# Performance work log

Measured on AMD Instinct MI355X. Metric: run time of the kernel, lower is better.

## Reference

```python
import jax, jax.numpy as jnp
import jax.scipy.linalg as jsl
import numpy as np

B, T, C = 2, 4096, 1024
HK = HV = 8           # linear_num_key_heads == linear_num_value_heads
DK = DV = 128         # linear_key_head_dim / linear_value_head_dim
CHUNK = 64
CONV_K = 4
KEY_DIM = HK * DK
VAL_DIM = HV * DV
CONV_DIM = 2 * KEY_DIM + VAL_DIM
EPS = 1e-6


def setup_inputs() -> dict:
    key = jax.random.key(0)
    ks = jax.random.split(key, 8)
    s = 0.02
    x = jax.random.normal(ks[0], (B, T, C), jnp.float32)
    W_qkvz = jax.random.normal(ks[1], (C, 2 * KEY_DIM + 2 * VAL_DIM), jnp.float32) * s
    W_ba = jax.random.normal(ks[2], (C, 2 * HV), jnp.float32) * s
    conv_w = jax.random.normal(ks[3], (CONV_DIM, 1, CONV_K), jnp.float32) * 0.3  # depthwise (O,1,K)
    dt_bias = jnp.ones((HV,), jnp.float32)
    A_log = jnp.log(jax.random.uniform(ks[4], (HV,), jnp.float32, 0.5, 8.0))
    norm_weight = jnp.ones((DV,), jnp.float32)
    W_out = jax.random.normal(ks[5], (VAL_DIM, C), jnp.float32) * s
    return {"x": x, "W_qkvz": W_qkvz, "W_ba": W_ba, "conv_w": conv_w,
            "dt_bias": dt_bias, "A_log": A_log, "norm_weight": norm_weight, "W_out": W_out}


def _l2norm(x, eps=EPS):
    return x * jax.lax.rsqrt(jnp.sum(x * x, -1, keepdims=True) + eps)


def _chunk_gated_delta_rule(q, k, v, g, beta, chunk=CHUNK):
    # q,k: (B,T,H,DK); v: (B,T,H,DV); g,beta: (B,T,H)
    q = _l2norm(q)
    k = _l2norm(k)
    tr = lambda x: jnp.swapaxes(x, 1, 2).astype(jnp.float32)  # -> (B,H,T,...)
    q, k, v, g, beta = tr(q), tr(k), tr(v), tr(g), tr(beta)
    b, h, t, dk = k.shape
    dv = v.shape[-1]
    n = t // chunk  # T divisible by chunk (pad_size == 0)
    q = q * (dk ** -0.5)
    v_beta = v * beta[..., None]
    k_beta = k * beta[..., None]
    rs = lambda x: x.reshape(b, h, n, chunk, x.shape[-1])
    q, k, v_beta, k_beta = rs(q), rs(k), rs(v_beta), rs(k_beta)
    g = jnp.cumsum(g.reshape(b, h, n, chunk), axis=-1)
    # decay_mask[..., i, j] = exp(g_i - g_j) for j <= i, else 0
    decay = jnp.tril(jnp.exp(jnp.tril(g[..., :, None] - g[..., None, :])))
    # forward substitution == unit-lower-triangular solve: (I + tri)^{-1}
    tri = jnp.tril(jnp.einsum('bhnck,bhndk->bhncd', k_beta, k) * decay, -1)
    eye = jnp.eye(chunk, dtype=jnp.float32)
    Tm = jsl.solve_triangular(eye + tri, jnp.broadcast_to(eye, tri.shape), lower=True)
    v_new = Tm @ v_beta                                   # (B,H,N,C,DV)
    k_cum = Tm @ (k_beta * jnp.exp(g)[..., None])         # (B,H,N,C,DK)
    keep_low = jnp.tril(jnp.ones((chunk, chunk), bool))

    def step(S, inp):
        q_i, k_i, v_i, kc_i, g_i, dm_i = inp              # (B,H,C,*)
        attn = jnp.where(keep_low, (q_i @ jnp.swapaxes(k_i, -1, -2)) * dm_i, 0.0)
        v_n = v_i - kc_i @ S
        out = (q_i * jnp.exp(g_i)[..., None]) @ S + attn @ v_n
        g_last = g_i[..., -1]
        S = S * jnp.exp(g_last)[..., None, None] + jnp.einsum(
            'bhck,bhcv->bhkv', k_i * jnp.exp(g_last[..., None] - g_i)[..., None], v_n)
        return S, out

    mv = lambda x: jnp.moveaxis(x, 2, 0)                  # chunk axis to front
    S0 = jnp.zeros((b, h, dk, dv), jnp.float32)
    S, outs = jax.lax.scan(step, S0, (mv(q), mv(k), mv(v_new), mv(k_cum), mv(g), mv(decay)))
    out = jnp.moveaxis(outs, 0, 2).reshape(b, h, t, dv)
    return jnp.swapaxes(out, 1, 2), S                     # (B,T,H,DV), (B,H,DK,DV)


def reference(x, W_qkvz, W_ba, conv_w, dt_bias, A_log, norm_weight, W_out):
    Bx, Tx, Cx = x.shape
    ratio = HV // HK
    qkvz = (x @ W_qkvz).reshape(Bx, Tx, HK, 2 * DK + 2 * ratio * DV)
    q, k, v, z = jnp.split(qkvz, [DK, 2 * DK, 2 * DK + ratio * DV], axis=3)
    v = v.reshape(Bx, Tx, HV, DV)
    z = z.reshape(Bx, Tx, HV, DV)
    ba = (x @ W_ba).reshape(Bx, Tx, HK, 2 * ratio)
    b_, a_ = jnp.split(ba, [ratio], axis=3)
    b_ = b_.reshape(Bx, Tx, HV)
    a_ = a_.reshape(Bx, Tx, HV)
    mixed = jnp.concatenate([q.reshape(Bx, Tx, -1), k.reshape(Bx, Tx, -1),
                             v.reshape(Bx, Tx, -1)], axis=-1)
    # causal depthwise conv1d (left pad K-1, take first T)
    xc = jnp.swapaxes(mixed, 1, 2)                        # (B, CONV_DIM, T)
    conv = jax.lax.conv_general_dilated(xc, conv_w, (1,), [(CONV_K - 1, 0)],
                                        dimension_numbers=('NCH', 'OIH', 'NCH'),
                                        feature_group_count=CONV_DIM)
    conv = jnp.swapaxes(jax.nn.silu(conv), 1, 2)          # (B,T,CONV_DIM)
    qc, kc, vc = jnp.split(conv, [KEY_DIM, 2 * KEY_DIM], axis=-1)
    qc = qc.reshape(Bx, Tx, HK, DK)
    kc = kc.reshape(Bx, Tx, HK, DK)
    vc = vc.reshape(Bx, Tx, HV, DV)
    if ratio > 1:
        qc = jnp.repeat(qc, ratio, axis=2)
        kc = jnp.repeat(kc, ratio, axis=2)
    beta = jax.nn.sigmoid(b_)
    g = -jnp.exp(A_log) * jax.nn.softplus(a_ + dt_bias)
    core, _ = _chunk_gated_delta_rule(qc, kc, vc, g, beta)
    # GatedRMSNorm over head_v_dim, gated by silu(z)
    h = core.astype(jnp.float32)
    var = jnp.mean(h * h, -1, keepdims=True)
    h = norm_weight * (h * jax.lax.rsqrt(var + EPS))
    h = h * jax.nn.silu(z.astype(jnp.float32))
    return h.reshape(Bx, Tx, VAL_DIM) @ W_out
```

## Files before the change

kernel.cpp:

```cpp
#include <hip/hip_runtime.h>
#include <cstddef>

#define Bx 2
#define Tn 4096
#define Hh 8

typedef unsigned short u16;
typedef unsigned int u32;
typedef __attribute__((ext_vector_type(8))) short short8;
typedef __attribute__((ext_vector_type(4))) float f32x4;

__device__ __forceinline__ float bf2f(u16 u) {
  u32 x = ((u32)u) << 16;
  return __uint_as_float(x);
}
__device__ __forceinline__ u16 f2bf(float f) {
  u32 x = __float_as_uint(f);
  u32 lsb = (x >> 16) & 1;
  x += 0x7fffu + lsb;
  return (u16)(x >> 16);
}
__device__ __forceinline__ u32 pack2(float a, float b) {
  return (u32)f2bf(a) | ((u32)f2bf(b) << 16);
}
__device__ __forceinline__ short8 cvt8(float4 f0, float4 f1) {
  uint4 p;
  p.x = pack2(f0.x, f0.y);
  p.y = pack2(f0.z, f0.w);
  p.z = pack2(f1.x, f1.y);
  p.w = pack2(f1.z, f1.w);
  return *(short8*)&p;
}
__device__ __forceinline__ void async16(u16* lds, const u16* g) {
  __builtin_amdgcn_global_load_lds((const __attribute__((address_space(1))) void*)g,
                                   (__attribute__((address_space(3))) void*)lds, 16, 0, 0);
}

__global__ __launch_bounds__(256) void conv_bf16(const float* __restrict__ X,
                                                 u16* __restrict__ Xb) {
  int i = (blockIdx.x * 256 + threadIdx.x) * 8;
  float4 v0 = *(const float4*)&X[i];
  float4 v1 = *(const float4*)&X[i + 4];
  uint4 pv;
  pv.x = pack2(v0.x, v0.y);
  pv.y = pack2(v0.z, v0.w);
  pv.z = pack2(v1.x, v1.y);
  pv.w = pack2(v1.z, v1.w);
  *(uint4*)&Xb[i] = pv;
}

__global__ __launch_bounds__(256) void transpose_bf16(const float* __restrict__ W,
                                                      u16* __restrict__ WT,
                                                      int K, int N) {
  __shared__ float tile[64][68];
  int nb = blockIdx.x, kb = blockIdx.y;
  int tid = threadIdx.x;
  int r = tid >> 4, c4 = (tid & 15) * 4;
#pragma unroll
  for (int p = 0; p < 4; p++) {
    int k = kb * 64 + p * 16 + r;
    float4 v = *(const float4*)&W[(size_t)k * N + nb * 64 + c4];
    tile[p * 16 + r][c4] = v.x;
    tile[p * 16 + r][c4 + 1] = v.y;
    tile[p * 16 + r][c4 + 2] = v.z;
    tile[p * 16 + r][c4 + 3] = v.w;
  }
  __syncthreads();
  int rn = tid >> 2, ck = (tid & 3) * 16;
#pragma unroll
  for (int s = 0; s < 2; s++) {
    int k0 = ck + s * 8;
    uint4 pv;
    pv.x = pack2(tile[k0 + 0][rn], tile[k0 + 1][rn]);
    pv.y = pack2(tile[k0 + 2][rn], tile[k0 + 3][rn]);
    pv.z = pack2(tile[k0 + 4][rn], tile[k0 + 5][rn]);
    pv.w = pack2(tile[k0 + 6][rn], tile[k0 + 7][rn]);
    *(uint4*)&WT[(size_t)(nb * 64 + rn) * K + kb * 64 + k0] = pv;
  }
}

__global__ __launch_bounds__(512, 1) void gemm_qkvz(const u16* __restrict__ A,
                                                    const u16* __restrict__ Bt,
                                                    u16* __restrict__ O1,
                                                    u16* __restrict__ O2) {
  const int K = 1024;
  extern __shared__ __align__(16) u16 gl[];
  int lin = blockIdx.x;
  int sl = (lin & 7) * 64 + (lin >> 3);
  int bm = sl & 31;
  int bn = sl >> 5;
  int tid = threadIdx.x;
  int wid = tid >> 6, lane = tid & 63;
  int wm = wid >> 2, wn = wid & 3;
  int m_lane = lane & 15, kgrp = lane >> 4, m7 = m_lane & 7;

  f32x4 acc[8][4];
#pragma unroll
  for (int i = 0; i < 8; i++)
#pragma unroll
    for (int j = 0; j < 4; j++) acc[i][j] = (f32x4){0.f, 0.f, 0.f, 0.f};

  int srow = lane >> 3;
  int gc8 = ((lane & 7) ^ srow) * 8;
  const u16* Ab = A + (size_t)(bm * 256 + wid * 32 + srow) * K + gc8;
  const u16* Bb = Bt + (size_t)(bn * 256 + wid * 32 + srow) * K + gc8;

#pragma unroll
  for (int i = 0; i < 4; i++) {
    async16(gl + (wid * 32 + i * 8) * 64, Ab + (size_t)(i * 8) * K);
    async16(gl + 32768 + (wid * 32 + i * 8) * 64, Bb + (size_t)(i * 8) * K);
  }
  asm volatile("s_waitcnt vmcnt(0)" ::: "memory");
  __builtin_amdgcn_s_barrier();

  for (int t = 0; t < 16; t++) {
    int p = t & 1;
    const u16* Ap = gl + p * 16384;
    const u16* Bp = gl + 32768 + p * 16384;
    if (t < 15) {
      int pn = p ^ 1;
      int kk = (t + 1) * 64;
#pragma unroll
      for (int i = 0; i < 4; i++) {
        async16(gl + pn * 16384 + (wid * 32 + i * 8) * 64, Ab + (size_t)(i * 8) * K + kk);
        async16(gl + 32768 + pn * 16384 + (wid * 32 + i * 8) * 64, Bb + (size_t)(i * 8) * K + kk);
      }
    }
    short8 bq[2][4];
#pragma unroll
    for (int ks = 0; ks < 2; ks++)
#pragma unroll
      for (int nf = 0; nf < 4; nf++)
        bq[ks][nf] = *(const short8*)&Bp[(wn * 64 + nf * 16 + m_lane) * 64 +
                                         (((ks * 4 + kgrp) ^ m7) << 3)];
#pragma unroll
    for (int mf = 0; mf < 8; mf++) {
      short8 aq0 = *(const short8*)&Ap[(wm * 128 + mf * 16 + m_lane) * 64 +
                                       ((kgrp ^ m7) << 3)];
      short8 aq1 = *(const short8*)&Ap[(wm * 128 + mf * 16 + m_lane) * 64 +
                                       (((4 + kgrp) ^ m7) << 3)];
#pragma unroll
      for (int nf = 0; nf < 4; nf++)
        acc[mf][nf] = __builtin_amdgcn_mfma_f32_16x16x32_bf16(aq0, bq[0][nf], acc[mf][nf], 0, 0, 0);
#pragma unroll
      for (int nf = 0; nf < 4; nf++)
        acc[mf][nf] = __builtin_amdgcn_mfma_f32_16x16x32_bf16(aq1, bq[1][nf], acc[mf][nf], 0, 0, 0);
    }
    if (t < 15) {
      asm volatile("s_waitcnt vmcnt(0) lgkmcnt(0)" ::: "memory");
      __builtin_amdgcn_s_barrier();
      __builtin_amdgcn_sched_barrier(0);
    }
  }

  int n0w = bn * 256 + wn * 64;
  int h = n0w >> 9, sub = (n0w >> 7) & 3;
  int cin = ((n0w & 127) & 64) + m_lane;
  u16* dst;
  size_t stride;
  if (sub < 3) { dst = O1 + (size_t)(sub * 1024 + h * 128); stride = 3072; }
  else         { dst = O2 + (size_t)(h * 128);              stride = 1024; }
  int rbase = bm * 256 + wm * 128 + kgrp * 4;
#pragma unroll
  for (int mf = 0; mf < 8; mf++)
#pragma unroll
    for (int nf = 0; nf < 4; nf++)
#pragma unroll
      for (int r = 0; r < 4; r++)
        dst[(size_t)(rbase + mf * 16 + r) * stride + cin + nf * 16] = f2bf(acc[mf][nf][r]);
}

template<int EPI>
__global__ __launch_bounds__(256) void gemm_mfma(const u16* __restrict__ A,
                                                 const u16* __restrict__ Bt,
                                                 u16* __restrict__ O1,
                                                 u16* __restrict__ O2,
                                                 float* __restrict__ O3,
                                                 int Nfull) {
  const int K = 1024;
  __shared__ u16 As[128 * 64];
  __shared__ u16 Bs[128 * 64];
  int lin = blockIdx.y * gridDim.x + blockIdx.x;
  int sl = lin >> 3;
  int cbn = gridDim.x >> 3;
  int bn = (lin & 7) * cbn + (sl % cbn);
  int bm = sl / cbn;
  int tid = threadIdx.x;
  int wave = tid >> 6, lane = tid & 63;
  int wr = wave >> 1, wc = wave & 1;

  f32x4 acc[4][4];
#pragma unroll
  for (int i = 0; i < 4; i++)
#pragma unroll
    for (int j = 0; j < 4; j++) acc[i][j] = (f32x4){0.f, 0.f, 0.f, 0.f};

  int srow = lane >> 3;
  int gc8 = ((lane & 7) ^ srow) * 8;
  const u16* Ab = A + (size_t)(bm * 128 + wave * 32 + srow) * K + gc8;
  const u16* Bb = Bt + (size_t)(bn * 128 + wave * 32 + srow) * K + gc8;
  u16* AsW = &As[(wave * 32) * 64];
  u16* BsW = &Bs[(wave * 32) * 64];

  int m_lane = lane & 15, kgrp = lane >> 4;
  int m7 = m_lane & 7;

  for (int kk = 0; kk < K; kk += 64) {
    __syncthreads();
#pragma unroll
    for (int i = 0; i < 4; i++) {
      async16(AsW + i * 512, Ab + (size_t)(i * 8) * K + kk);
      async16(BsW + i * 512, Bb + (size_t)(i * 8) * K + kk);
    }
    __syncthreads();
    short8 a[4][2], b[4][2];
#pragma unroll
    for (int t = 0; t < 4; t++)
#pragma unroll
      for (int ks = 0; ks < 2; ks++) {
        a[t][ks] = *(const short8*)&As[(wr * 64 + t * 16 + m_lane) * 64 +
                                       (((ks * 4 + kgrp) ^ m7) << 3)];
        b[t][ks] = *(const short8*)&Bs[(wc * 64 + t * 16 + m_lane) * 64 +
                                       (((ks * 4 + kgrp) ^ m7) << 3)];
      }
#pragma unroll
    for (int ks = 0; ks < 2; ks++)
#pragma unroll
      for (int i = 0; i < 4; i++)
#pragma unroll
        for (int j = 0; j < 4; j++)
          acc[i][j] = __builtin_amdgcn_mfma_f32_16x16x32_bf16(a[i][ks], b[j][ks],
                                                              acc[i][j], 0, 0, 0);
  }

  int n0 = bn * 128;
  int cbase = wc * 64 + (lane & 15);
  int rbase = bm * 128 + wr * 64 + ((lane >> 4) * 4);
  if (EPI == 1) {
    int h = n0 >> 9, sub = (n0 >> 7) & 3;
    u16* dst;
    size_t stride;
    if (sub < 3) { dst = O1 + (size_t)(sub * 1024 + h * 128); stride = 3072; }
    else         { dst = O2 + (size_t)(h * 128);              stride = 1024; }
#pragma unroll
    for (int i = 0; i < 4; i++)
#pragma unroll
      for (int j = 0; j < 4; j++)
#pragma unroll
        for (int r = 0; r < 4; r++)
          dst[(size_t)(rbase + i * 16 + r) * stride + cbase + j * 16] = f2bf(acc[i][j][r]);
  } else {
#pragma unroll
    for (int i = 0; i < 4; i++)
#pragma unroll
      for (int j = 0; j < 4; j++)
#pragma unroll
        for (int r = 0; r < 4; r++)
          O3[(size_t)(rbase + i * 16 + r) * Nfull + n0 + cbase + j * 16] = acc[i][j][r];
  }
}

__global__ __launch_bounds__(128) void ba_kernel(const float* __restrict__ x,
                                                 const float* __restrict__ Wba,
                                                 const float* __restrict__ dtb,
                                                 const float* __restrict__ Alog,
                                                 float* __restrict__ betab,
                                                 float* __restrict__ gb) {
  __shared__ float xs[1024];
  __shared__ float part[8][16];
  int row = blockIdx.x, tid = threadIdx.x;
#pragma unroll
  for (int r = 0; r < 2; r++) {
    int f4 = r * 128 + tid;
    *(float4*)&xs[f4 * 4] = *(const float4*)&x[(size_t)row * 1024 + f4 * 4];
  }
  __syncthreads();
  int col = tid & 15, seg = tid >> 4;
  float a = 0.f;
  for (int k = seg * 128; k < seg * 128 + 128; k++) a += xs[k] * Wba[k * 16 + col];
  part[seg][col] = a;
  __syncthreads();
  if (tid < 8) {
    float bval = 0.f, aval = 0.f;
#pragma unroll
    for (int q = 0; q < 8; q++) { bval += part[q][tid * 2]; aval += part[q][tid * 2 + 1]; }
    betab[(size_t)row * 8 + tid] = 1.f / (1.f + expf(-bval));
    float spin = aval + dtb[tid];
    float sp = (spin > 20.f) ? spin : log1pf(expf(spin));
    gb[(size_t)row * 8 + tid] = -expf(Alog[tid]) * sp;
  }
}

__global__ __launch_bounds__(256) void convnorm(const u16* __restrict__ mixed,
                                                const float* __restrict__ cw,
                                                const float* __restrict__ gbuf,
                                                u16* __restrict__ qn,
                                                u16* __restrict__ kn,
                                                u16* __restrict__ kdT,
                                                u16* __restrict__ vbT) {
  __shared__ __align__(16) u16 sRaw[67 * 128];
  __shared__ __align__(16) u16 sO[64 * 136];
  __shared__ float red_s[256];
  __shared__ float inv_s[64];
  __shared__ float eglc_s[64];
  int n = blockIdx.x, bh = blockIdx.y, type = blockIdx.z;
  int b = bh >> 3, h = bh & 7;
  int t0 = n * 64, tid = threadIdx.x;
  int srow = tid >> 4, scol8 = (tid & 15) * 8;
  int base = type << 10;

#pragma unroll
  for (int pass = 0; pass < 5; pass++) {
    int r = pass * 16 + srow;
    if (r < 67) {
      int t = t0 - 3 + r;
      uint4 v = make_uint4(0u, 0u, 0u, 0u);
      if (t >= 0) v = *(const uint4*)&mixed[(size_t)(b * Tn + t) * 3072 + base + h * 128 + scol8];
      *(uint4*)&sRaw[r * 128 + scol8] = v;
    }
  }
  if (type == 1 && tid < 64) {
    float gv = gbuf[(size_t)(b * Tn + t0 + tid) * 8 + h];
#pragma unroll
    for (int off = 1; off < 64; off <<= 1) {
      float o = __shfl_up(gv, off, 64);
      if (tid >= off) gv += o;
    }
    float gl = __shfl(gv, 63, 64);
    eglc_s[tid] = expf(gl - gv);
  }
  __syncthreads();

#pragma unroll
  for (int it = 0; it < 32; it++) {
    int idx = it * 256 + tid;
    int i = idx >> 7, d = idx & 127;
    int colw = (base + h * 128 + d) * 4;
    float a = 0.f;
#pragma unroll
    for (int tap = 0; tap < 4; tap++)
      a += bf2f(sRaw[(i + tap) * 128 + d]) * cw[colw + tap];
    a = a / (1.f + expf(-a));
    sO[i * 136 + d] = f2bf(a);
  }
  __syncthreads();

  if (type == 2) {
    const size_t tbase = (size_t)(bh * 64 + n) * 8192;
#pragma unroll
    for (int it = 0; it < 32; it++) {
      int idx = it * 256 + tid;
      int d = idx >> 6, i = idx & 63;
      vbT[tbase + d * 64 + i] = sO[i * 136 + d];
    }
    return;
  }

  {
    int i = tid >> 2, p = tid & 3;
    float ss = 0.f;
#pragma unroll
    for (int d = p * 32; d < p * 32 + 32; d += 2) {
      u32 w2 = *(const u32*)&sO[i * 136 + d];
      float a = bf2f(w2 & 0xffff), b2 = bf2f(w2 >> 16);
      ss += a * a + b2 * b2;
    }
    red_s[tid] = ss;
  }
  __syncthreads();
  if (tid < 64) {
    float inv = rsqrtf(red_s[tid * 4] + red_s[tid * 4 + 1] + red_s[tid * 4 + 2] + red_s[tid * 4 + 3] + 1e-6f);
    inv_s[tid] = (type == 0) ? inv * 0.08838834764831845f : inv;
  }
  __syncthreads();
  u16* dstRow = (type == 0 ? qn : kn) + (size_t)(bh * Tn + t0) * 128;
#pragma unroll
  for (int it = 0; it < 16; it++) {
    int idx = it * 256 + tid;
    int i = idx >> 6, d2 = (idx & 63) * 2;
    u32 w2 = *(const u32*)&sO[i * 136 + d2];
    float inv = inv_s[i];
    float q0 = bf2f(w2 & 0xffff) * inv, q1 = bf2f(w2 >> 16) * inv;
    u32 pk = pack2(q0, q1);
    if (type == 1) *(u32*)&sO[i * 136 + d2] = pk;
    *(u32*)&dstRow[(size_t)i * 128 + d2] = pk;
  }
  if (type == 1) {
    __syncthreads();
    const size_t tbase = (size_t)(bh * 64 + n) * 8192;
#pragma unroll
    for (int it = 0; it < 32; it++) {
      int idx = it * 256 + tid;
      int d = idx >> 6, i = idx & 63;
      kdT[tbase + d * 64 + i] = f2bf(bf2f(sO[i * 136 + d]) * eglc_s[i]);
    }
  }
}

__global__ __launch_bounds__(256) void prep(const float* __restrict__ gbuf,
                                            const float* __restrict__ betabuf,
                                            u16* qbuf,
                                            u16* kbuf,
                                            u16* vnT,
                                            u16* __restrict__ attn,
                                            float* __restrict__ egl) {
  __shared__ __align__(16) u16 sKn[64 * 136];
  __shared__ __align__(16) u16 sQn[64 * 136];
  __shared__ float gc_s[64], egc_s[64], bet_s[64];
  float* triL = (float*)sQn;

  int n = blockIdx.x, bh = blockIdx.y;
  int b = bh >> 3, h = bh & 7;
  int t0 = n * 64;
  int tid = threadIdx.x;
  const int rowg0 = b * Tn + t0;
  const int rowh0 = bh * Tn + t0;
  const size_t tbase = (size_t)(bh * 64 + n) * 8192;

  int wv = tid >> 6, lane = tid & 63;
  int m16 = lane & 15, q8 = (lane >> 4) * 8, qr = (lane >> 4) * 4;

#pragma unroll
  for (int it = 0; it < 4; it++) {
    int idx = it * 256 + tid;
    int i = idx >> 4, c8 = (idx & 15) * 8;
    *(uint4*)&sQn[i * 136 + c8] = *(const uint4*)&qbuf[(size_t)(rowh0 + i) * 128 + c8];
    *(uint4*)&sKn[i * 136 + c8] = *(const uint4*)&kbuf[(size_t)(rowh0 + i) * 128 + c8];
  }
  if (tid < 64) {
    float gv = gbuf[(size_t)(rowg0 + tid) * 8 + h];
    float bv = betabuf[(size_t)(rowg0 + tid) * 8 + h];
#pragma unroll
    for (int off = 1; off < 64; off <<= 1) {
      float o = __shfl_up(gv, off, 64);
      if (tid >= off) gv += o;
    }
    float gl = __shfl(gv, 63, 64);
    gc_s[tid] = gv;
    egc_s[tid] = expf(gv);
    bet_s[tid] = bv;
    if (tid == 63) egl[bh * 64 + n] = expf(gl);
  }
  __syncthreads();

#pragma unroll
  for (int it = 0; it < 16; it++) {
    int idx = it * 256 + tid;
    int i = idx >> 6, d2 = (idx & 63) * 2;
    u32 w2 = *(const u32*)&sQn[i * 136 + d2];
    float e = egc_s[i];
    *(u32*)&qbuf[(size_t)(rowh0 + i) * 128 + d2] =
        pack2(bf2f(w2 & 0xffff) * e, bf2f(w2 >> 16) * e);
  }
  {
    short8 qa[4];
#pragma unroll
    for (int kt = 0; kt < 4; kt++)
      qa[kt] = *(const short8*)&sQn[(wv * 16 + m16) * 136 + kt * 32 + q8];
    u16* atp = attn + (size_t)(bh * 64 + n) * 4096;
#pragma unroll
    for (int jt = 0; jt < 4; jt++) {
      int j = jt * 16 + m16;
      if (jt <= wv) {
        f32x4 o = (f32x4){0.f, 0.f, 0.f, 0.f};
#pragma unroll
        for (int kt = 0; kt < 4; kt++) {
          short8 kb = *(const short8*)&sKn[(jt * 16 + m16) * 136 + kt * 32 + q8];
          o = __builtin_amdgcn_mfma_f32_16x16x32_bf16(qa[kt], kb, o, 0, 0, 0);
        }
#pragma unroll
        for (int r = 0; r < 4; r++) {
          int i = wv * 16 + qr + r;
          float val = (j <= i) ? o[r] * expf(gc_s[i] - gc_s[j]) : 0.f;
          atp[i * 64 + j] = f2bf(val);
        }
      } else {
#pragma unroll
        for (int r = 0; r < 4; r++) atp[(wv * 16 + qr + r) * 64 + j] = 0;
      }
    }
  }
  __syncthreads();
  {
    short8 ka[4];
#pragma unroll
    for (int kt = 0; kt < 4; kt++)
      ka[kt] = *(const short8*)&sKn[(wv * 16 + m16) * 136 + kt * 32 + q8];
#pragma unroll
    for (int jt = 0; jt < 4; jt++) {
      int j = jt * 16 + m16;
      if (jt <= wv) {
        f32x4 o = (f32x4){0.f, 0.f, 0.f, 0.f};
#pragma unroll
        for (int kt = 0; kt < 4; kt++) {
          short8 kb = *(const short8*)&sKn[(jt * 16 + m16) * 136 + kt * 32 + q8];
          o = __builtin_amdgcn_mfma_f32_16x16x32_bf16(ka[kt], kb, o, 0, 0, 0);
        }
#pragma unroll
        for (int r = 0; r < 4; r++) {
          int i = wv * 16 + qr + r;
          triL[i * 64 + j] = (j < i) ? bet_s[i] * expf(gc_s[i] - gc_s[j]) * o[r] : 0.f;
        }
      } else if (jt == wv + 1) {
#pragma unroll
        for (int r = 0; r < 4; r++) triL[(wv * 16 + qr + r) * 64 + j] = 0.f;
      }
    }
  }
  __syncthreads();

  {
    int mat = tid >> 7, c = tid & 127;
    float x[64];
    if (mat == 0) {
#pragma unroll
      for (int i = 0; i < 64; i++)
        x[i] = bf2f(sKn[i * 136 + c]) * bet_s[i] * egc_s[i];
    } else {
#pragma unroll
      for (int i8 = 0; i8 < 8; i8++) {
        short8 vv = *(const short8*)&vnT[tbase + c * 64 + i8 * 8];
#pragma unroll
        for (int j = 0; j < 8; j++)
          x[i8 * 8 + j] = bf2f((u16)vv[j]) * bet_s[i8 * 8 + j];
      }
    }
#pragma unroll
    for (int i = 1; i < 64; i++) {
      float s0 = 0.f, s1 = 0.f, s2 = 0.f, s3 = 0.f;
#pragma unroll
      for (int l4 = 0; l4 < (i + 3) / 4; l4++) {
        float4 t4 = *(float4*)&triL[i * 64 + l4 * 4];
        s0 += t4.x * x[l4 * 4 + 0];
        s1 += t4.y * x[l4 * 4 + 1];
        s2 += t4.z * x[l4 * 4 + 2];
        s3 += t4.w * x[l4 * 4 + 3];
      }
      x[i] = x[i] - ((s0 + s1) + (s2 + s3));
    }
    if (mat == 0) {
#pragma unroll
      for (int i = 0; i < 64; i++) kbuf[(size_t)(rowh0 + i) * 128 + c] = f2bf(-x[i]);
    } else {
#pragma unroll
      for (int i = 0; i < 64; i += 2)
        *(u32*)&vnT[tbase + c * 64 + i] = pack2(x[i], x[i + 1]);
    }
  }
}

__device__ __forceinline__ void stage_quarter(int w, u16* ldsb,
                                              const u16* __restrict__ qgc,
                                              const u16* __restrict__ kcc,
                                              const u16* __restrict__ ktc,
                                              const u16* __restrict__ atc,
                                              const u16* __restrict__ vtc,
                                              int lane) {
  int l8 = lane * 8;
  if (w == 0) {
#pragma unroll
    for (int i = 0; i < 16; i++) {
      int p = i * 512 + l8;
      async16(ldsb + 8192 + i * 512, kcc + (p ^ ((((p >> 7) & 15)) << 3)));
    }
  } else if (w == 1) {
#pragma unroll
    for (int i = 0; i < 16; i++) {
      int p = i * 512 + l8;
      async16(ldsb + 16384 + i * 512, ktc + (p ^ ((((p >> 6) & 7)) << 3)));
    }
  } else if (w == 2) {
#pragma unroll
    for (int i = 0; i < 16; i++) {
      int p = i * 512 + l8;
      async16(ldsb + i * 512, qgc + (p ^ ((((p >> 7) & 15)) << 3)));
    }
  } else {
#pragma unroll
    for (int i = 0; i < 8; i++) {
      int p = i * 512 + l8;
      async16(ldsb + 24576 + i * 512, atc + (p ^ ((((p >> 6) & 7)) << 3)));
    }
#pragma unroll
    for (int i = 0; i < 2; i++) {
      int p = i * 512 + l8;
      async16(ldsb + 28672 + i * 512, vtc + (p ^ ((((p >> 6) & 7)) << 3)));
    }
  }
}

__global__ __launch_bounds__(256, 1) void scan_mfma(const u16* __restrict__ qg,
                                                    const u16* __restrict__ kdT,
                                                    const u16* __restrict__ vnT,
                                                    const u16* __restrict__ kcum,
                                                    const u16* __restrict__ attn,
                                                    const float* __restrict__ egl,
                                                    float* __restrict__ core) {
  extern __shared__ __align__(16) u16 dyn[];
  __shared__ __align__(16) u16 STb[16 * 128];
  __shared__ __align__(16) u16 VNb[16 * 64];
  int blk = blockIdx.x;
  int bh = blk & 15, tile = blk >> 4;
  int dv0 = tile * 16;
  int b = bh >> 3, h = bh & 7;
  int tid = threadIdx.x;
  int w = tid >> 6, lane = tid & 63;
  int q = lane >> 4, col = lane & 15;
  int c7 = col & 7;
  int qh = q >> 1, ql = q & 1;

  for (int r = tid; r < 16 * 128 / 2; r += 256) ((u32*)STb)[r] = 0u;
  float egAll = egl[bh * 64 + lane];

  f32x4 st0 = (f32x4){0.f, 0.f, 0.f, 0.f};
  f32x4 st1 = (f32x4){0.f, 0.f, 0.f, 0.f};

  const u16* qg_base = qg + (size_t)bh * Tn * 128;
  const u16* kc_base = kcum + (size_t)bh * Tn * 128;
  const u16* kt_base = kdT + (size_t)bh * 64 * 8192;
  const u16* at_base = attn + (size_t)bh * 64 * 4096;
  const u16* vt_base = vnT + (size_t)bh * 64 * 8192 + dv0 * 64;

  stage_quarter(w, dyn, qg_base, kc_base, kt_base, at_base, vt_base, lane);
  asm volatile("s_waitcnt vmcnt(0)" ::: "memory");
  __syncthreads();

  for (int n = 0; n < 64; n++) {
    u16* buf = dyn + (n & 1) * 29696;

    short8 kcf[4], qgf[4], ktf[4], atf[2], sb[4];
    uint2 vtf;
#pragma unroll
    for (int kt = 0; kt < 4; kt++) {
      kcf[kt] = *(const short8*)&buf[8192 + (w * 16 + col) * 128 + (((kt * 4 + q) ^ col) << 3)];
      qgf[kt] = *(const short8*)&buf[(w * 16 + col) * 128 + (((kt * 4 + q) ^ col) << 3)];
      sb[kt] = *(const short8*)&STb[col * 128 + (((kt * 4 + q) ^ col) << 3)];
    }
#pragma unroll
    for (int kt2 = 0; kt2 < 2; kt2++) {
      atf[kt2] = *(const short8*)&buf[24576 + (w * 16 + col) * 64 + (((kt2 * 4 + q) ^ c7) << 3)];
#pragma unroll
      for (int t = 0; t < 2; t++)
        ktf[t * 2 + kt2] = *(const short8*)&buf[16384 + ((w * 2 + t) * 16 + col) * 64 +
                                                (((kt2 * 4 + q) ^ c7) << 3)];
    }
    vtf = *(const uint2*)&buf[28672 + col * 64 + (((w * 2 + qh) ^ c7) << 3) + ql * 4];

    if (n < 63) {
      stage_quarter(w, dyn + ((n + 1) & 1) * 29696,
                    qg_base + (size_t)(n + 1) * 8192,
                    kc_base + (size_t)(n + 1) * 8192,
                    kt_base + (size_t)(n + 1) * 8192,
                    at_base + (size_t)(n + 1) * 4096,
                    vt_base + (size_t)(n + 1) * 8192, lane);
    }
    float eg = __shfl(egAll, n, 64);

    {
      f32x4 a0;
      a0[0] = bf2f(vtf.x & 0xffff); a0[1] = bf2f(vtf.x >> 16);
      a0[2] = bf2f(vtf.y & 0xffff); a0[3] = bf2f(vtf.y >> 16);
#pragma unroll
      for (int kt = 0; kt < 4; kt++)
        a0 = __builtin_amdgcn_mfma_f32_16x16x32_bf16(kcf[kt], sb[kt], a0, 0, 0, 0);
      uint2 pk;
      pk.x = pack2(a0[0], a0[1]);
      pk.y = pack2(a0[2], a0[3]);
      *(uint2*)&VNb[col * 64 + (((w * 2 + qh) ^ c7) << 3) + ql * 4] = pk;
    }
    asm volatile("s_waitcnt lgkmcnt(0)" ::: "memory");
    __builtin_amdgcn_s_barrier();
    __builtin_amdgcn_sched_barrier(0);

    short8 vb[2];
#pragma unroll
    for (int kt2 = 0; kt2 < 2; kt2++)
      vb[kt2] = *(const short8*)&VNb[col * 64 + (((kt2 * 4 + q) ^ c7) << 3)];

    {
      f32x4 s0;
      s0[0] = st0[0] * eg; s0[1] = st0[1] * eg; s0[2] = st0[2] * eg; s0[3] = st0[3] * eg;
      s0 = __builtin_amdgcn_mfma_f32_16x16x32_bf16(ktf[0], vb[0], s0, 0, 0, 0);
      s0 = __builtin_amdgcn_mfma_f32_16x16x32_bf16(ktf[1], vb[1], s0, 0, 0, 0);
      st0 = s0;
      uint2 pk;
      pk.x = pack2(s0[0], s0[1]);
      pk.y = pack2(s0[2], s0[3]);
      *(uint2*)&STb[col * 128 + ((((w * 2 + 0) * 2 + qh) ^ col) << 3) + ql * 4] = pk;
    }
    {
      f32x4 s1;
      s1[0] = st1[0] * eg; s1[1] = st1[1] * eg; s1[2] = st1[2] * eg; s1[3] = st1[3] * eg;
      s1 = __builtin_amdgcn_mfma_f32_16x16x32_bf16(ktf[2], vb[0], s1, 0, 0, 0);
      s1 = __builtin_amdgcn_mfma_f32_16x16x32_bf16(ktf[3], vb[1], s1, 0, 0, 0);
      st1 = s1;
      uint2 pk;
      pk.x = pack2(s1[0], s1[1]);
      pk.y = pack2(s1[2], s1[3]);
      *(uint2*)&STb[col * 128 + ((((w * 2 + 1) * 2 + qh) ^ col) << 3) + ql * 4] = pk;
    }

    {
      f32x4 o = (f32x4){0.f, 0.f, 0.f, 0.f};
#pragma unroll
      for (int kt = 0; kt < 4; kt++)
        o = __builtin_amdgcn_mfma_f32_16x16x32_bf16(qgf[kt], sb[kt], o, 0, 0, 0);
#pragma unroll
      for (int kt2 = 0; kt2 < 2; kt2++)
        o = __builtin_amdgcn_mfma_f32_16x16x32_bf16(atf[kt2], vb[kt2], o, 0, 0, 0);
      size_t rowb = (size_t)(b * Tn) + n * 64 + w * 16 + q * 4;
#pragma unroll
      for (int r2 = 0; r2 < 4; r2++)
        core[(rowb + r2) * 1024 + h * 128 + dv0 + col] = o[r2];
    }

    asm volatile("s_waitcnt vmcnt(4) lgkmcnt(0)" ::: "memory");
    __builtin_amdgcn_s_barrier();
    __builtin_amdgcn_sched_barrier(0);
  }
}

__global__ __launch_bounds__(256) void gnorm(const float* __restrict__ core,
                                             const u16* __restrict__ z,
                                             const float* __restrict__ nw,
                                             u16* __restrict__ coreb) {
  __shared__ float red[256];
  __shared__ float rstd[8];
  int row = blockIdx.x, tid = threadIdx.x;
  float4 c4 = *(const float4*)&core[(size_t)row * 1024 + tid * 4];
  uint2 zl = *(const uint2*)&z[(size_t)row * 1024 + tid * 4];
  float4 z4;
  z4.x = bf2f(zl.x & 0xffff); z4.y = bf2f(zl.x >> 16);
  z4.z = bf2f(zl.y & 0xffff); z4.w = bf2f(zl.y >> 16);
  red[tid] = c4.x * c4.x + c4.y * c4.y + c4.z * c4.z + c4.w * c4.w;
  __syncthreads();
  if (tid < 8) {
    float s = 0.f;
    for (int t2 = tid * 32; t2 < tid * 32 + 32; t2++) s += red[t2];
    rstd[tid] = rsqrtf(s * (1.f / 128.f) + 1e-6f);
  }
  __syncthreads();
  float rs = rstd[tid >> 5];
  int d0 = (tid * 4) & 127;
  float4 w4 = *(const float4*)&nw[d0];
  float4 o;
  o.x = c4.x * rs * w4.x * (z4.x / (1.f + expf(-z4.x)));
  o.y = c4.y * rs * w4.y * (z4.y / (1.f + expf(-z4.y)));
  o.z = c4.z * rs * w4.z * (z4.z / (1.f + expf(-z4.z)));
  o.w = c4.w * rs * w4.w * (z4.w / (1.f + expf(-z4.w)));
  uint2 pv;
  pv.x = pack2(o.x, o.y);
  pv.y = pack2(o.z, o.w);
  *(uint2*)&coreb[(size_t)row * 1024 + tid * 4] = pv;
}

extern "C" void kernel_launch(void* const* d_in, const int* in_sizes, int n_in,
                              void* d_out, int out_size, void* d_ws, size_t ws_size,
                              hipStream_t stream) {
  const float* x     = (const float*)d_in[0];
  const float* Wqkvz = (const float*)d_in[1];
  const float* Wba   = (const float*)d_in[2];
  const float* convw = (const float*)d_in[3];
  const float* dtb   = (const float*)d_in[4];
  const float* Alog  = (const float*)d_in[5];
  const float* nw    = (const float*)d_in[6];
  const float* Wout  = (const float*)d_in[7];
  float* out = (float*)d_out;

  char* w = (char*)d_ws;
  u16*   mixed = (u16*)w;
  float* core  = (float*)w;
  u16*   coreb = (u16*)(w + 33554432);
  u16*   zb    = (u16*)(w + 50331648);
  float* betab = (float*)(w + 67108864);
  float* gb    = (float*)(w + 67371008);
  u16*   qgB   = (u16*)(w + 67633152);
  u16*   xb    = (u16*)(w + 67633152);
  u16*   kdTB  = (u16*)(w + 84410368);
  u16*   WqT   = (u16*)(w + 84410368);
  u16*   vnTB  = (u16*)(w + 101187584);
  u16*   kcB   = (u16*)(w + 117964800);
  u16*   WoT   = (u16*)(w + 117964800);
  u16*   atB   = (u16*)(w + 134742016);
  float* eglB  = (float*)(w + 143130624);

  static bool attr_set = false;
  if (!attr_set) {
    hipFuncSetAttribute(reinterpret_cast<const void*>(scan_mfma),
                        hipFuncAttributeMaxDynamicSharedMemorySize, 118784);
    hipFuncSetAttribute(reinterpret_cast<const void*>(gemm_qkvz),
                        hipFuncAttributeMaxDynamicSharedMemorySize, 131072);
    attr_set = true;
  }

  conv_bf16<<<dim3(4096), 256, 0, stream>>>(x, xb);
  transpose_bf16<<<dim3(64, 16), 256, 0, stream>>>(Wqkvz, WqT, 1024, 4096);
  gemm_qkvz<<<dim3(512), 512, 131072, stream>>>(xb, WqT, mixed, zb);
  ba_kernel<<<dim3(8192), 128, 0, stream>>>(x, Wba, dtb, Alog, betab, gb);
  convnorm<<<dim3(64, 16, 3), 256, 0, stream>>>(mixed, convw, gb, qgB, kcB, kdTB, vnTB);
  prep<<<dim3(64, 16), 256, 0, stream>>>(gb, betab, qgB, kcB, vnTB, atB, eglB);
  scan_mfma<<<dim3(128), 256, 118784, stream>>>(qgB, kdTB, vnTB, kcB, atB, eglB, core);
  transpose_bf16<<<dim3(16, 16), 256, 0, stream>>>(Wout, WoT, 1024, 1024);
  gnorm<<<dim3(8192), 256, 0, stream>>>(core, zb, nw, coreb);
  gemm_mfma<0><<<dim3(8, 64), 256, 0, stream>>>(coreb, WoT, nullptr, nullptr, out, 1024);
}
```

Measured before the change: 394.4 us.

## Process two DV tiles per scan block to reuse staged q/k/attn loads

Each scan_mfma block now handles two 16-wide value-dim tiles instead of one. The shared q, kcum, kdT and attn chunks staged into LDS serve both tiles, and the grid drops from 128 to 64 blocks. This halves redundant global and LDS traffic per unit of work. The cost is fewer blocks in flight on a GPU with many CUs, which lowers parallelism for this latency-bound sequential scan, and each block carries twice the MFMA work per chunk.

Result: slower. 423.0 us (+7.2%).

```diff
diff --git a/kernel.cpp b/kernel.cpp
--- a/kernel.cpp
+++ b/kernel.cpp
@@ -549,13 +549,14 @@
   }
 }
 
-__device__ __forceinline__ void stage_quarter(int w, u16* ldsb,
-                                              const u16* __restrict__ qgc,
-                                              const u16* __restrict__ kcc,
-                                              const u16* __restrict__ ktc,
-                                              const u16* __restrict__ atc,
-                                              const u16* __restrict__ vtc,
-                                              int lane) {
+__device__ __forceinline__ void stage_pair(int w, u16* ldsb,
+                                           const u16* __restrict__ qgc,
+                                           const u16* __restrict__ kcc,
+                                           const u16* __restrict__ ktc,
+                                           const u16* __restrict__ atc,
+                                           const u16* __restrict__ vtA,
+                                           const u16* __restrict__ vtB,
+                                           int lane) {
   int l8 = lane * 8;
   if (w == 0) {
 #pragma unroll
@@ -584,7 +585,12 @@
 #pragma unroll
     for (int i = 0; i < 2; i++) {
       int p = i * 512 + l8;
-      async16(ldsb + 28672 + i * 512, vtc + (p ^ ((((p >> 6) & 7)) << 3)));
+      async16(ldsb + 28672 + i * 512, vtA + (p ^ ((((p >> 6) & 7)) << 3)));
+    }
+#pragma unroll
+    for (int i = 0; i < 2; i++) {
+      int p = i * 512 + l8;
+      async16(ldsb + 29696 + i * 512, vtB + (p ^ ((((p >> 6) & 7)) << 3)));
     }
   }
 }
@@ -597,11 +603,13 @@
                                                     const float* __restrict__ egl,
                                                     float* __restrict__ core) {
   extern __shared__ __align__(16) u16 dyn[];
-  __shared__ __align__(16) u16 STb[16 * 128];
-  __shared__ __align__(16) u16 VNb[16 * 64];
+  __shared__ __align__(16) u16 STbA[16 * 128];
+  __shared__ __align__(16) u16 STbB[16 * 128];
+  __shared__ __align__(16) u16 VNbA[16 * 64];
+  __shared__ __align__(16) u16 VNbB[16 * 64];
   int blk = blockIdx.x;
-  int bh = blk & 15, tile = blk >> 4;
-  int dv0 = tile * 16;
+  int bh = blk & 15, pair = blk >> 4;
+  int dv0 = pair * 32;
   int b = bh >> 3, h = bh & 7;
   int tid = threadIdx.x;
   int w = tid >> 6, lane = tid & 63;
@@ -609,32 +617,39 @@
   int c7 = col & 7;
   int qh = q >> 1, ql = q & 1;
 
-  for (int r = tid; r < 16 * 128 / 2; r += 256) ((u32*)STb)[r] = 0u;
+  for (int r = tid; r < 16 * 128 / 2; r += 256) {
+    ((u32*)STbA)[r] = 0u;
+    ((u32*)STbB)[r] = 0u;
+  }
   float egAll = egl[bh * 64 + lane];
 
-  f32x4 st0 = (f32x4){0.f, 0.f, 0.f, 0.f};
-  f32x4 st1 = (f32x4){0.f, 0.f, 0.f, 0.f};
+  f32x4 stA0 = (f32x4){0.f, 0.f, 0.f, 0.f};
+  f32x4 stA1 = (f32x4){0.f, 0.f, 0.f, 0.f};
+  f32x4 stB0 = (f32x4){0.f, 0.f, 0.f, 0.f};
+  f32x4 stB1 = (f32x4){0.f, 0.f, 0.f, 0.f};
 
   const u16* qg_base = qg + (size_t)bh * Tn * 128;
   const u16* kc_base = kcum + (size_t)bh * Tn * 128;
   const u16* kt_base = kdT + (size_t)bh * 64 * 8192;
   const u16* at_base = attn + (size_t)bh * 64 * 4096;
-  const u16* vt_base = vnT + (size_t)bh * 64 * 8192 + dv0 * 64;
-
-  stage_quarter(w, dyn, qg_base, kc_base, kt_base, at_base, vt_base, lane);
+  const u16* vtA_base = vnT + (size_t)bh * 64 * 8192 + dv0 * 64;
+  const u16* vtB_base = vtA_base + 1024;
+
+  stage_pair(w, dyn, qg_base, kc_base, kt_base, at_base, vtA_base, vtB_base, lane);
   asm volatile("s_waitcnt vmcnt(0)" ::: "memory");
   __syncthreads();
 
   for (int n = 0; n < 64; n++) {
-    u16* buf = dyn + (n & 1) * 29696;
-
-    short8 kcf[4], qgf[4], ktf[4], atf[2], sb[4];
-    uint2 vtf;
+    u16* buf = dyn + (n & 1) * 30720;
+
+    short8 kcf[4], qgf[4], ktf[4], atf[2], sbA[4], sbB[4];
+    uint2 vtfA, vtfB;
 #pragma unroll
     for (int kt = 0; kt < 4; kt++) {
       kcf[kt] = *(const short8*)&buf[8192 + (w * 16 + col) * 128 + (((kt * 4 + q) ^ col) << 3)];
       qgf[kt] = *(const short8*)&buf[(w * 16 + col) * 128 + (((kt * 4 + q) ^ col) << 3)];
-      sb[kt] = *(const short8*)&STb[col * 128 + (((kt * 4 + q) ^ col) << 3)];
+      sbA[kt] = *(const short8*)&STbA[col * 128 + (((kt * 4 + q) ^ col) << 3)];
+      sbB[kt] = *(const short8*)&STbB[col * 128 + (((kt * 4 + q) ^ col) << 3)];
     }
 #pragma unroll
     for (int kt2 = 0; kt2 < 2; kt2++) {
@@ -644,77 +659,107 @@
         ktf[t * 2 + kt2] = *(const short8*)&buf[16384 + ((w * 2 + t) * 16 + col) * 64 +
                                                 (((kt2 * 4 + q) ^ c7) << 3)];
     }
-    vtf = *(const uint2*)&buf[28672 + col * 64 + (((w * 2 + qh) ^ c7) << 3) + ql * 4];
+    vtfA = *(const uint2*)&buf[28672 + col * 64 + (((w * 2 + qh) ^ c7) << 3) + ql * 4];
+    vtfB = *(const uint2*)&buf[29696 + col * 64 + (((w * 2 + qh) ^ c7) << 3) + ql * 4];
 
     if (n < 63) {
-      stage_quarter(w, dyn + ((n + 1) & 1) * 29696,
-                    qg_base + (size_t)(n + 1) * 8192,
-                    kc_base + (size_t)(n + 1) * 8192,
-                    kt_base + (size_t)(n + 1) * 8192,
-                    at_base + (size_t)(n + 1) * 4096,
-                    vt_base + (size_t)(n + 1) * 8192, lane);
+      stage_pair(w, dyn + ((n + 1) & 1) * 30720,
+                 qg_base + (size_t)(n + 1) * 8192,
+                 kc_base + (size_t)(n + 1) * 8192,
+                 kt_base + (size_t)(n + 1) * 8192,
+                 at_base + (size_t)(n + 1) * 4096,
+                 vtA_base + (size_t)(n + 1) * 8192,
+                 vtB_base + (size_t)(n + 1) * 8192, lane);
     }
     float eg = __shfl(egAll, n, 64);
 
     {
-      f32x4 a0;
-      a0[0] = bf2f(vtf.x & 0xffff); a0[1] = bf2f(vtf.x >> 16);
-      a0[2] = bf2f(vtf.y & 0xffff); a0[3] = bf2f(vtf.y >> 16);
-#pragma unroll
-      for (int kt = 0; kt < 4; kt++)
-        a0 = __builtin_amdgcn_mfma_f32_16x16x32_bf16(kcf[kt], sb[kt], a0, 0, 0, 0);
-      uint2 pk;
-      pk.x = pack2(a0[0], a0[1]);
-      pk.y = pack2(a0[2], a0[3]);
-      *(uint2*)&VNb[col * 64 + (((w * 2 + qh) ^ c7) << 3) + ql * 4] = pk;
+      f32x4 aA, aB;
+      aA[0] = bf2f(vtfA.x & 0xffff); aA[1] = bf2f(vtfA.x >> 16);
+      aA[2] = bf2f(vtfA.y & 0xffff); aA[3] = bf2f(vtfA.y >> 16);
+      aB[0] = bf2f(vtfB.x & 0xffff); aB[1] = bf2f(vtfB.x >> 16);
+      aB[2] = bf2f(vtfB.y & 0xffff); aB[3] = bf2f(vtfB.y >> 16);
+#pragma unroll
+      for (int kt = 0; kt < 4; kt++) {
+        aA = __builtin_amdgcn_mfma_f32_16x16x32_bf16(kcf[kt], sbA[kt], aA, 0, 0, 0);
+        aB = __builtin_amdgcn_mfma_f32_16x16x32_bf16(kcf[kt], sbB[kt], aB, 0, 0, 0);
+      }
+      uint2 pkA, pkB;
+      pkA.x = pack2(aA[0], aA[1]); pkA.y = pack2(aA[2], aA[3]);
+      pkB.x = pack2(aB[0], aB[1]); pkB.y = pack2(aB[2], aB[3]);
+      *(uint2*)&VNbA[col * 64 + (((w * 2 + qh) ^ c7) << 3) + ql * 4] = pkA;
+      *(uint2*)&VNbB[col * 64 + (((w * 2 + qh) ^ c7) << 3) + ql * 4] = pkB;
     }
     asm volatile("s_waitcnt lgkmcnt(0)" ::: "memory");
     __builtin_amdgcn_s_barrier();
     __builtin_amdgcn_sched_barrier(0);
 
-    short8 vb[2];
-#pragma unroll
-    for (int kt2 = 0; kt2 < 2; kt2++)
-      vb[kt2] = *(const short8*)&VNb[col * 64 + (((kt2 * 4 + q) ^ c7) << 3)];
+    short8 vbA[2], vbB[2];
+#pragma unroll
+    for (int kt2 = 0; kt2 < 2; kt2++) {
+      vbA[kt2] = *(const short8*)&VNbA[col * 64 + (((kt2 * 4 + q) ^ c7) << 3)];
+      vbB[kt2] = *(const short8*)&VNbB[col * 64 + (((kt2 * 4 + q) ^ c7) << 3)];
+    }
 
     {
-      f32x4 s0;
-      s0[0] = st0[0] * eg; s0[1] = st0[1] * eg; s0[2] = st0[2] * eg; s0[3] = st0[3] * eg;
-      s0 = __builtin_amdgcn_mfma_f32_16x16x32_bf16(ktf[0], vb[0], s0, 0, 0, 0);
-      s0 = __builtin_amdgcn_mfma_f32_16x16x32_bf16(ktf[1], vb[1], s0, 0, 0, 0);
-      st0 = s0;
-      uint2 pk;
-      pk.x = pack2(s0[0], s0[1]);
-      pk.y = pack2(s0[2], s0[3]);
-      *(uint2*)&STb[col * 128 + ((((w * 2 + 0) * 2 + qh) ^ col) << 3) + ql * 4] = pk;
+      f32x4 s;
+      s[0] = stA0[0] * eg; s[1] = stA0[1] * eg; s[2] = stA0[2] * eg; s[3] = stA0[3] * eg;
+      s = __builtin_amdgcn_mfma_f32_16x16x32_bf16(ktf[0], vbA[0], s, 0, 0, 0);
+      s = __builtin_amdgcn_mfma_f32_16x16x32_bf16(ktf[1], vbA[1], s, 0, 0, 0);
+      stA0 = s;
+      uint2 pk; pk.x = pack2(s[0], s[1]); pk.y = pack2(s[2], s[3]);
+      *(uint2*)&STbA[col * 128 + ((((w * 2 + 0) * 2 + qh) ^ col) << 3) + ql * 4] = pk;
     }
     {
-      f32x4 s1;
-      s1[0] = st1[0] * eg; s1[1] = st1[1] * eg; s1[2] = st1[2] * eg; s1[3] = st1[3] * eg;
-      s1 = __builtin_amdgcn_mfma_f32_16x16x32_bf16(ktf[2], vb[0], s1, 0, 0, 0);
-      s1 = __builtin_amdgcn_mfma_f32_16x16x32_bf16(ktf[3], vb[1], s1, 0, 0, 0);
-      st1 = s1;
-      uint2 pk;
-      pk.x = pack2(s1[0], s1[1]);
-      pk.y = pack2(s1[2], s1[3]);
-      *(uint2*)&STb[col * 128 + ((((w * 2 + 1) * 2 + qh) ^ col) << 3) + ql * 4] = pk;
-    }
-
+      f32x4 s;
+      s[0] = stB0[0] * eg; s[1] = stB0[1] * eg; s[2] = stB0[2] * eg; s[3] = stB0[3] * eg;
+      s = __builtin_amdgcn_mfma_f32_16x16x32_bf16(ktf[0], vbB[0], s, 0, 0, 0);
+      s = __builtin_amdgcn_mfma_f32_16x16x32_bf16(ktf[1], vbB[1], s, 0, 0, 0);
+      stB0 = s;
+      uint2 pk; pk.x = pack2(s[0], s[1]); pk.y = pack2(s[2], s[3]);
+      *(uint2*)&STbB[col * 128 + ((((w * 2 + 0) * 2 + qh) ^ col) << 3) + ql * 4] = pk;
+    }
     {
-      f32x4 o = (f32x4){0.f, 0.f, 0.f, 0.f};
-#pragma unroll
-      for (int kt = 0; kt < 4; kt++)
-        o = __builtin_amdgcn_mfma_f32_16x16x32_bf16(qgf[kt], sb[kt], o, 0, 0, 0);
-#pragma unroll
-      for (int kt2 = 0; kt2 < 2; kt2++)
-        o = __builtin_amdgcn_mfma_f32_16x16x32_bf16(atf[kt2], vb[kt2], o, 0, 0, 0);
+      f32x4 s;
+      s[0] = stA1[0] * eg; s[1] = stA1[1] * eg; s[2] = stA1[2] * eg; s[3] = stA1[3] * eg;
+      s = __builtin_amdgcn_mfma_f32_16x16x32_bf16(ktf[2], vbA[0], s, 0, 0, 0);
+      s = __builtin_amdgcn_mfma_f32_16x16x32_bf16(ktf[3], vbA[1], s, 0, 0, 0);
+      stA1 = s;
+      uint2 pk; pk.x = pack2(s[0], s[1]); pk.y = pack2(s[2], s[3]);
+      *(uint2*)&STbA[col * 128 + ((((w * 2 + 1) * 2 + qh) ^ col) << 3) + ql * 4] = pk;
+    }
+    {
+      f32x4 s;
+      s[0] = stB1[0] * eg; s[1] = stB1[1] * eg; s[2] = stB1[2] * eg; s[3] = stB1[3] * eg;
+      s = __builtin_amdgcn_mfma_f32_16x16x32_bf16(ktf[2], vbB[0], s, 0, 0, 0);
+      s = __builtin_amdgcn_mfma_f32_16x16x32_bf16(ktf[3], vbB[1], s, 0, 0, 0);
+      stB1 = s;
+      uint2 pk; pk.x = pack2(s[0], s[1]); pk.y = pack2(s[2], s[3]);
+      *(uint2*)&STbB[col * 128 + ((((w * 2 + 1) * 2 + qh) ^ col) << 3) + ql * 4] = pk;
+    }
+
+    {
+      f32x4 oA = (f32x4){0.f, 0.f, 0.f, 0.f};
+      f32x4 oB = (f32x4){0.f, 0.f, 0.f, 0.f};
+#pragma unroll
+      for (int kt = 0; kt < 4; kt++) {
+        oA = __builtin_amdgcn_mfma_f32_16x16x32_bf16(qgf[kt], sbA[kt], oA, 0, 0, 0);
+        oB = __builtin_amdgcn_mfma_f32_16x16x32_bf16(qgf[kt], sbB[kt], oB, 0, 0, 0);
+      }
+#pragma unroll
+      for (int kt2 = 0; kt2 < 2; kt2++) {
+        oA = __builtin_amdgcn_mfma_f32_16x16x32_bf16(atf[kt2], vbA[kt2], oA, 0, 0, 0);
+        oB = __builtin_amdgcn_mfma_f32_16x16x32_bf16(atf[kt2], vbB[kt2], oB, 0, 0, 0);
+      }
       size_t rowb = (size_t)(b * Tn) + n * 64 + w * 16 + q * 4;
 #pragma unroll
-      for (int r2 = 0; r2 < 4; r2++)
-        core[(rowb + r2) * 1024 + h * 128 + dv0 + col] = o[r2];
-    }
-
-    asm volatile("s_waitcnt vmcnt(4) lgkmcnt(0)" ::: "memory");
+      for (int r2 = 0; r2 < 4; r2++) {
+        core[(rowb + r2) * 1024 + h * 128 + dv0 + col] = oA[r2];
+        core[(rowb + r2) * 1024 + h * 128 + dv0 + 16 + col] = oB[r2];
+      }
+    }
+
+    asm volatile("s_waitcnt vmcnt(8) lgkmcnt(0)" ::: "memory");
     __builtin_amdgcn_s_barrier();
     __builtin_amdgcn_sched_barrier(0);
   }
@@ -787,7 +832,7 @@
   static bool attr_set = false;
   if (!attr_set) {
     hipFuncSetAttribute(reinterpret_cast<const void*>(scan_mfma),
-                        hipFuncAttributeMaxDynamicSharedMemorySize, 118784);
+                        hipFuncAttributeMaxDynamicSharedMemorySize, 122880);
     hipFuncSetAttribute(reinterpret_cast<const void*>(gemm_qkvz),
                         hipFuncAttributeMaxDynamicSharedMemorySize, 131072);
     attr_set = true;
@@ -799,7 +844,7 @@
   ba_kernel<<<dim3(8192), 128, 0, stream>>>(x, Wba, dtb, Alog, betab, gb);
   convnorm<<<dim3(64, 16, 3), 256, 0, stream>>>(mixed, convw, gb, qgB, kcB, kdTB, vnTB);
   prep<<<dim3(64, 16), 256, 0, stream>>>(gb, betab, qgB, kcB, vnTB, atB, eglB);
-  scan_mfma<<<dim3(128), 256, 118784, stream>>>(qgB, kdTB, vnTB, kcB, atB, eglB, core);
+  scan_mfma<<<dim3(64), 256, 122880, stream>>>(qgB, kdTB, vnTB, kcB, atB, eglB, core);
   transpose_bf16<<<dim3(16, 16), 256, 0, stream>>>(Wout, WoT, 1024, 1024);
   gnorm<<<dim3(8192), 256, 0, stream>>>(core, zb, nw, coreb);
   gemm_mfma<0><<<dim3(8, 64), 256, 0, stream>>>(coreb, WoT, nullptr, nullptr, out, 1024);
```
